# Optimization experiments

Hardware: AMD Instinct MI355X
Metric: run time of the kernel (lower is better)

## Reference

```python
import jax, jax.numpy as jnp
import numpy as np

INPUT_SIZE = 512
HIDDEN_SIZE = 4096
OUTPUT_SIZE = 512
BATCH = 16384

def _xavier_uniform(key, shape):
    fan_out, fan_in = shape
    limit = np.sqrt(6.0 / (fan_in + fan_out)).astype(np.float32)
    return jax.random.uniform(key, shape, jnp.float32, -limit, limit)

def setup_inputs() -> dict:
    key = jax.random.key(0)
    kx, kk, kg = jax.random.split(key, 3)
    x = jax.random.normal(kx, (BATCH, INPUT_SIZE), dtype=jnp.float32)
    kohonen_weights = _xavier_uniform(kk, (HIDDEN_SIZE, INPUT_SIZE))
    grossberg_weights = _xavier_uniform(kg, (OUTPUT_SIZE, HIDDEN_SIZE))
    return {"x": x, "kohonen_weights": kohonen_weights, "grossberg_weights": grossberg_weights}

def reference(x, kohonen_weights, grossberg_weights):
    # cdist (euclidean): sq distances suffice for argmin; sqrt kept for faithfulness
    x_sq = jnp.sum(x * x, axis=1, keepdims=True)                # [B,1]
    w_sq = jnp.sum(kohonen_weights * kohonen_weights, axis=1)   # [H]
    sq = x_sq - 2.0 * (x @ kohonen_weights.T) + w_sq[None, :]   # [B,H]
    distances = jnp.sqrt(jnp.maximum(sq, 0.0))
    winner_indices = jnp.argmin(distances, axis=1)              # [B]
    # one-hot @ grossberg.T == gather rows of grossberg.T
    output = jnp.take(grossberg_weights.T, winner_indices, axis=0)  # [B,O]
    return (output, winner_indices)
```

## Files before the change

kernel.cpp:

```cpp
#include <hip/hip_runtime.h>
#include <cstdint>
#include <cstddef>

#define B_ 16384
#define K_ 512
#define H_ 4096
#define O_ 512

typedef __attribute__((ext_vector_type(4))) float f32x4;
typedef __attribute__((ext_vector_type(8))) short bf16x8;

#define EPS_FLAG 0.125f

__device__ inline unsigned short f32_to_bf16_rne(float f) {
  unsigned u = __float_as_uint(f);
  unsigned r = (u + 0x7fffu + ((u >> 16) & 1u)) >> 16;
  return (unsigned short)r;
}

__device__ float np_pairwise_sumsq512(const float* __restrict__ a) {
  float s[4];
  #pragma unroll
  for (int blk = 0; blk < 4; ++blk) {
    const float* p = a + blk * 128;
    float r[8];
    #pragma unroll
    for (int j = 0; j < 8; ++j) r[j] = __fmul_rn(p[j], p[j]);
    for (int i = 8; i < 128; i += 8) {
      #pragma unroll
      for (int j = 0; j < 8; ++j) r[j] = __fadd_rn(r[j], __fmul_rn(p[i + j], p[i + j]));
    }
    s[blk] = __fadd_rn(__fadd_rn(__fadd_rn(r[0], r[1]), __fadd_rn(r[2], r[3])),
                       __fadd_rn(__fadd_rn(r[4], r[5]), __fadd_rn(r[6], r[7])));
  }
  return __fadd_rn(__fadd_rn(s[0], s[1]), __fadd_rn(s[2], s[3]));
}

__global__ __launch_bounds__(256) void prep_all_kernel(
    const float* __restrict__ x, const float* __restrict__ W,
    const float* __restrict__ G,
    unsigned short* __restrict__ xhi, unsigned short* __restrict__ whi,
    float* __restrict__ xsq, float* __restrict__ wsq, float* __restrict__ GT) {
  const int bid = (int)blockIdx.x;
  const int tid = (int)threadIdx.x;

  if (bid < 2560) {
    const float* src = bid < 2048 ? x : W;
    unsigned short* hi = bid < 2048 ? xhi : whi;
    float* sumsq = bid < 2048 ? xsq : wsq;
    const int r0 = (bid < 2048 ? bid : bid - 2048) * 8;

    __shared__ float buf[8 * 512];
    #pragma unroll
    for (int it = 0; it < 4; ++it) {
      int i = tid + it * 256;
      float4 v = ((const float4*)(src + (size_t)r0 * K_))[i];
      ((float4*)buf)[i] = v;
      ushort4 h;
      h.x = f32_to_bf16_rne(v.x);
      h.y = f32_to_bf16_rne(v.y);
      h.z = f32_to_bf16_rne(v.z);
      h.w = f32_to_bf16_rne(v.w);
      ((ushort4*)(hi + (size_t)r0 * K_))[i] = h;
    }
    __syncthreads();

    const int row = tid >> 5, l = tid & 31, blk = l >> 3, j = l & 7;
    const float* p = buf + row * 512 + blk * 128;
    float r = __fmul_rn(p[j], p[j]);
    #pragma unroll
    for (int i = 8; i < 128; i += 8) r = __fadd_rn(r, __fmul_rn(p[i + j], p[i + j]));
    r = __fadd_rn(r, __shfl_xor(r, 1));
    r = __fadd_rn(r, __shfl_xor(r, 2));
    r = __fadd_rn(r, __shfl_xor(r, 4));
    r = __fadd_rn(r, __shfl_xor(r, 8));
    r = __fadd_rn(r, __shfl_xor(r, 16));
    if (l == 0) sumsq[r0 + row] = r;
  } else {
    __shared__ float t[32][33];
    const int bid2 = bid - 2560;
    const int h0 = (bid2 & 127) * 32, o0 = (bid2 >> 7) * 32;
    const int tx = tid & 31, ty = tid >> 5;
    for (int i = ty; i < 32; i += 8)
      t[i][tx] = G[(size_t)(o0 + i) * H_ + h0 + tx];
    __syncthreads();
    for (int i = ty; i < 32; i += 8)
      GT[(size_t)(h0 + i) * O_ + o0 + tx] = t[tx][i];
  }
}

__global__ void rowsumsq_kernel(const float* __restrict__ src, float* __restrict__ dst,
                                int nrows) {
  int r = blockIdx.x * blockDim.x + threadIdx.x;
  if (r < nrows) dst[r] = np_pairwise_sumsq512(src + (size_t)r * K_);
}

__global__ void transposeG_kernel(const float* __restrict__ G, float* __restrict__ GT) {
  __shared__ float t[32][33];
  int h0 = blockIdx.x * 32, o0 = blockIdx.y * 32;
  for (int i = threadIdx.y; i < 32; i += 8)
    t[i][threadIdx.x] = G[(size_t)(o0 + i) * H_ + h0 + threadIdx.x];
  __syncthreads();
  for (int i = threadIdx.y; i < 32; i += 8)
    GT[(size_t)(h0 + i) * O_ + o0 + threadIdx.x] = t[threadIdx.x][i];
}

__device__ inline void stage_panel256(char* lds_panel, const unsigned short* __restrict__ src,
                                      int rowbase, int kt, int tid) {
  #pragma unroll
  for (int j = 0; j < 4; ++j) {
    int u = j * 512 + tid;
    int row = u >> 3, slot = u & 7;
    const char* g = (const char*)src + (size_t)(rowbase + row) * (K_ * 2) + kt * 128 +
                    ((slot ^ (row & 7)) * 16);
    __builtin_amdgcn_global_load_lds((const __attribute__((address_space(1))) void*)g,
                                     (__attribute__((address_space(3))) void*)(lds_panel + u * 16),
                                     16, 0, 0);
  }
}

__global__ __launch_bounds__(512, 2) void phase1_mfma_kernel(
    const unsigned short* __restrict__ xhi, const unsigned short* __restrict__ whi,
    const float* __restrict__ wsq, const float* __restrict__ xsq,
    float* __restrict__ gmin16 ,
    unsigned short* __restrict__ mk16 ) {
  __shared__ __align__(16) char smem[131072];
  const int tid = (int)threadIdx.x;
  const int wid = tid >> 6, lane = tid & 63;
  const int wr = wid >> 2, wc = wid & 3;
  const int cb = blockIdx.y;
  const int row0 = blockIdx.x * 256, col0 = cb * 256;

  f32x4 acc[8][4];
  #pragma unroll
  for (int i = 0; i < 8; ++i)
    #pragma unroll
    for (int j = 0; j < 4; ++j) acc[i][j] = (f32x4){0.f, 0.f, 0.f, 0.f};

  const int r16 = lane & 15, r7 = lane & 7, sg = lane >> 4;
  const int offK0 = ((sg ^ r7) & 7) * 16;
  const int offK1 = (((4 + sg) ^ r7) & 7) * 16;
  const int arowb = wr * 128 + r16;
  const int browb = wc * 64 + r16;

  stage_panel256(smem, xhi, row0, 0, tid);
  stage_panel256(smem + 32768, whi, col0, 0, tid);
  __syncthreads();

  int buf = 0;
  for (int kt = 0; kt < 8; ++kt) {
    if (kt < 7) {
      stage_panel256(smem + (buf ^ 1) * 65536, xhi, row0, kt + 1, tid);
      stage_panel256(smem + (buf ^ 1) * 65536 + 32768, whi, col0, kt + 1, tid);
    }
    const char* A = smem + buf * 65536;
    const char* Bm = smem + buf * 65536 + 32768;
    #pragma unroll
    for (int ks = 0; ks < 2; ++ks) {
      const int offK = ks ? offK1 : offK0;
      bf16x8 ah[8];
      #pragma unroll
      for (int mf = 0; mf < 8; ++mf)
        ah[mf] = *(const bf16x8*)(A + (arowb + mf * 16) * 128 + offK);
      #pragma unroll
      for (int nf = 0; nf < 4; ++nf) {
        bf16x8 bh = *(const bf16x8*)(Bm + (browb + nf * 16) * 128 + offK);
        #pragma unroll
        for (int mf = 0; mf < 8; ++mf)
          acc[mf][nf] = __builtin_amdgcn_mfma_f32_16x16x32_bf16(ah[mf], bh, acc[mf][nf], 0, 0, 0);
      }
    }
    __syncthreads();
    buf ^= 1;
  }

  float* T = (float*)smem + wid * (16 * 129);
  float* EpiF = (float*)(smem + 66048);
  unsigned short* EpiM = (unsigned short*)(smem + 82432);

  const float xq0 = xsq[row0 + wr * 128 + lane];
  const float xq1 = xsq[row0 + wr * 128 + 64 + lane];
  const int c = r16;

  #pragma unroll
  for (int nf = 0; nf < 4; ++nf) {
    float wq = wsq[col0 + wc * 64 + nf * 16 + c];
    #pragma unroll
    for (int mf = 0; mf < 8; ++mf)
      #pragma unroll
      for (int r = 0; r < 4; ++r)
        T[c * 129 + mf * 16 + sg * 4 + r] = wq - 2.0f * acc[mf][nf][r];
    asm volatile("s_waitcnt lgkmcnt(0)" ::: "memory");
    __builtin_amdgcn_sched_barrier(0);
    #pragma unroll
    for (int half = 0; half < 2; ++half) {
      int lrow = lane + half * 64;
      float xq = half ? xq1 : xq0;
      float v[16];
      #pragma unroll
      for (int c2 = 0; c2 < 16; ++c2) v[c2] = T[c2 * 129 + lrow];
      float mn = v[0];
      #pragma unroll
      for (int c2 = 1; c2 < 16; ++c2) mn = fminf(mn, v[c2]);
      unsigned msk = 0;
      #pragma unroll
      for (int c2 = 0; c2 < 16; ++c2)
        if ((v[c2] <= mn + EPS_FLAG) || (v[c2] + xq <= EPS_FLAG)) msk |= 1u << c2;
      EpiF[(wr * 128 + lrow) * 16 + wc * 4 + nf] = mn;
      EpiM[(wr * 128 + lrow) * 16 + wc * 4 + nf] = (unsigned short)msk;
    }
  }
  __syncthreads();

  {
    int row = tid >> 1, hf = tid & 1;
    const float* fr = EpiF + row * 16 + hf * 8;
    size_t gbase = (size_t)(row0 + row) * 256 + cb * 16 + hf * 8;
    *(float4*)&gmin16[gbase] = *(const float4*)fr;
    *(float4*)&gmin16[gbase + 4] = *(const float4*)(fr + 4);
    uint4 mv = *(const uint4*)(EpiM + row * 16 + hf * 8);
    *(uint4*)&mk16[gbase] = mv;
  }
}

#define P2_ROWS 16
#define P2_CAP 2048

__global__ __launch_bounds__(256) void phase2_block_kernel(
    const float* __restrict__ gm ,
    const unsigned short* __restrict__ mk ,
    const float* __restrict__ x, const float* __restrict__ W,
    const float* __restrict__ xsq, const float* __restrict__ wsq,
    const float* __restrict__ GT, float* __restrict__ out) {
  __shared__ float xls[P2_ROWS * 516];
  __shared__ unsigned short clist[P2_CAP];
  __shared__ unsigned long long bestkey[P2_ROWS];
  __shared__ int ncand;
  const int tid = (int)threadIdx.x;
  const int r = tid >> 4, t16 = tid & 15;
  const int b0 = blockIdx.x * P2_ROWS;
  const int b = b0 + r;

  if (tid < P2_ROWS) bestkey[tid] = 0xFFFFFFFFFFFFFFFFULL;
  if (tid == 0) ncand = 0;

  #pragma unroll
  for (int it = 0; it < 8; ++it) {
    int idx = tid + it * 256;
    int xr = idx >> 7, xw = idx & 127;
    float4 v = ((const float4*)(x + (size_t)(b0 + xr) * K_))[xw];
    *(float4*)&xls[xr * 516 + xw * 4] = v;
  }

  float gv[16];
  #pragma unroll
  for (int j = 0; j < 4; ++j) {
    float4 v = *(const float4*)(gm + (size_t)b * 256 + t16 * 16 + j * 4);
    gv[j * 4 + 0] = v.x;
    gv[j * 4 + 1] = v.y;
    gv[j * 4 + 2] = v.z;
    gv[j * 4 + 3] = v.w;
  }
  unsigned short mv[16];
  #pragma unroll
  for (int j = 0; j < 2; ++j) {
    uint4 u = *(const uint4*)(mk + (size_t)b * 256 + t16 * 16 + j * 8);
    mv[j * 8 + 0] = (unsigned short)(u.x & 0xFFFF);
    mv[j * 8 + 1] = (unsigned short)(u.x >> 16);
    mv[j * 8 + 2] = (unsigned short)(u.y & 0xFFFF);
    mv[j * 8 + 3] = (unsigned short)(u.y >> 16);
    mv[j * 8 + 4] = (unsigned short)(u.z & 0xFFFF);
    mv[j * 8 + 5] = (unsigned short)(u.z >> 16);
    mv[j * 8 + 6] = (unsigned short)(u.w & 0xFFFF);
    mv[j * 8 + 7] = (unsigned short)(u.w >> 16);
  }

  float mn = gv[0];
  #pragma unroll
  for (int j = 1; j < 16; ++j) mn = fminf(mn, gv[j]);
  #pragma unroll
  for (int off = 1; off < 16; off <<= 1) mn = fminf(mn, __shfl_xor(mn, off, 16));
  const float xq = xsq[b];
  const float thr = mn + EPS_FLAG;
  __syncthreads();

  #pragma unroll
  for (int j = 0; j < 16; ++j) {
    float v = gv[j];
    if ((v <= thr) || (v + xq <= EPS_FLAG)) {
      int g = t16 * 16 + j;
      unsigned mbits = mv[j];
      while (mbits) {
        int bit = __ffs(mbits) - 1;
        mbits &= mbits - 1;
        int slot = atomicAdd(&ncand, 1);
        if (slot < P2_CAP)
          clist[slot] = (unsigned short)((r << 12) | (g * 16 + bit));
      }
    }
  }
  __syncthreads();

  int total = ncand;
  if (total <= P2_CAP) {
    for (int i = tid; i < total; i += 256) {
      unsigned e = clist[i];
      int rr = (int)(e >> 12);
      int col = (int)(e & 0xFFF);
      const float* xr = xls + rr * 516;
      const float4* wrow = (const float4*)(W + (size_t)col * K_);
      float acc = 0.0f;
      #pragma unroll 8
      for (int kq = 0; kq < K_ / 4; ++kq) {
        float4 xv = *(const float4*)&xr[kq * 4];
        float4 wv = wrow[kq];
        acc = fmaf(xv.x, wv.x, acc);
        acc = fmaf(xv.y, wv.y, acc);
        acc = fmaf(xv.z, wv.z, acc);
        acc = fmaf(xv.w, wv.w, acc);
      }
      float xqr = xsq[b0 + rr];
      float t2 = xqr - 2.0f * acc;
      float sq = t2 + wsq[col];
      float d = sqrtf(fmaxf(sq, 0.0f));
      unsigned long long key =
          ((unsigned long long)__float_as_uint(d) << 32) | (unsigned)col;
      atomicMin(&bestkey[rr], key);
    }
  } else {
    for (int cc = t16; cc < H_; cc += 16) {
      int g = cc >> 4;
      float gvv = gm[(size_t)b * 256 + g];
      if ((gvv <= thr || gvv + xq <= EPS_FLAG) &&
          ((mk[(size_t)b * 256 + g] >> (cc & 15)) & 1)) {
        const float* xr = xls + r * 516;
        const float4* wrow = (const float4*)(W + (size_t)cc * K_);
        float acc = 0.0f;
        #pragma unroll 8
        for (int kq = 0; kq < K_ / 4; ++kq) {
          float4 xv = *(const float4*)&xr[kq * 4];
          float4 wv = wrow[kq];
          acc = fmaf(xv.x, wv.x, acc);
          acc = fmaf(xv.y, wv.y, acc);
          acc = fmaf(xv.z, wv.z, acc);
          acc = fmaf(xv.w, wv.w, acc);
        }
        float t2 = xq - 2.0f * acc;
        float sq = t2 + wsq[cc];
        float d = sqrtf(fmaxf(sq, 0.0f));
        unsigned long long key =
            ((unsigned long long)__float_as_uint(d) << 32) | (unsigned)cc;
        atomicMin(&bestkey[r], key);
      }
    }
  }
  __syncthreads();

  {
    const unsigned h = (unsigned)(bestkey[r] & 0xFFFFFFFFULL);
    const float4* gsrc = (const float4*)(GT + (size_t)h * O_);
    float4* gdst = (float4*)(out + (size_t)b * O_);
    #pragma unroll
    for (int j = 0; j < 8; ++j) gdst[j * 16 + t16] = gsrc[j * 16 + t16];
    if (t16 == 0) out[(size_t)B_ * O_ + b] = (float)h;
  }
}

#define BM 128
#define BN 128
#define BKK 16

__global__ void init_keys_kernel(unsigned long long* __restrict__ keys) {
  int i = blockIdx.x * blockDim.x + threadIdx.x;
  if (i < B_) keys[i] = 0xFFFFFFFFFFFFFFFFULL;
}

__global__ __launch_bounds__(256) void dist_argmin_kernel(
    const float* __restrict__ x, const float* __restrict__ W,
    const float* __restrict__ xsq, const float* __restrict__ wsq,
    unsigned long long* __restrict__ keys) {
  __shared__ float xs[BKK][BM + 4];
  __shared__ float wsh[BKK][BN + 4];
  const int row0 = blockIdx.x * BM;
  const int col0 = blockIdx.y * BN;
  const int tid = (int)threadIdx.x;
  const int tx = tid & 15, ty = tid >> 4;

  float acc[8][8];
  #pragma unroll
  for (int i = 0; i < 8; ++i)
    #pragma unroll
    for (int j = 0; j < 8; ++j) acc[i][j] = 0.0f;

  for (int kt = 0; kt < K_; kt += BKK) {
    #pragma unroll
    for (int l = 0; l < 2; ++l) {
      int e = tid + l * 256;
      int r = e >> 2, kq = e & 3;
      float4 v = *(const float4*)(x + (size_t)(row0 + r) * K_ + kt + kq * 4);
      xs[kq * 4 + 0][r] = v.x;
      xs[kq * 4 + 1][r] = v.y;
      xs[kq * 4 + 2][r] = v.z;
      xs[kq * 4 + 3][r] = v.w;
      float4 u = *(const float4*)(W + (size_t)(col0 + r) * K_ + kt + kq * 4);
      wsh[kq * 4 + 0][r] = u.x;
      wsh[kq * 4 + 1][r] = u.y;
      wsh[kq * 4 + 2][r] = u.z;
      wsh[kq * 4 + 3][r] = u.w;
    }
    __syncthreads();
    #pragma unroll
    for (int k = 0; k < BKK; ++k) {
      float4 a0 = *(const float4*)&xs[k][ty * 4];
      float4 a1 = *(const float4*)&xs[k][ty * 4 + 64];
      float4 b0 = *(const float4*)&wsh[k][tx * 4];
      float4 b1 = *(const float4*)&wsh[k][tx * 4 + 64];
      float ar[8] = {a0.x, a0.y, a0.z, a0.w, a1.x, a1.y, a1.z, a1.w};
      float br[8] = {b0.x, b0.y, b0.z, b0.w, b1.x, b1.y, b1.z, b1.w};
      #pragma unroll
      for (int i = 0; i < 8; ++i)
        #pragma unroll
        for (int j = 0; j < 8; ++j)
          acc[i][j] = fmaf(ar[i], br[j], acc[i][j]);
    }
    __syncthreads();
  }

  float xv[8], wv[8];
  int rowidx[8], colidx[8];
  #pragma unroll
  for (int i = 0; i < 8; ++i) {
    rowidx[i] = row0 + ty * 4 + (i & 3) + (i >> 2) * 64;
    xv[i] = xsq[rowidx[i]];
  }
  #pragma unroll
  for (int j = 0; j < 8; ++j) {
    colidx[j] = col0 + tx * 4 + (j & 3) + (j >> 2) * 64;
    wv[j] = wsq[colidx[j]];
  }
  #pragma unroll
  for (int i = 0; i < 8; ++i) {
    unsigned long long best = 0xFFFFFFFFFFFFFFFFULL;
    #pragma unroll
    for (int j = 0; j < 8; ++j) {
      float t2 = xv[i] - 2.0f * acc[i][j];
      float sq = t2 + wv[j];
      float d = sqrtf(fmaxf(sq, 0.0f));
      unsigned long long key =
          ((unsigned long long)__float_as_uint(d) << 32) | (unsigned)colidx[j];
      best = key < best ? key : best;
    }
    #pragma unroll
    for (int off = 1; off < 16; off <<= 1) {
      unsigned long long o = __shfl_xor(best, off, 16);
      best = o < best ? o : best;
    }
    if (tx == 0) atomicMin(&keys[rowidx[i]], best);
  }
}

__global__ void finalize_kernel(const unsigned long long* __restrict__ keys,
                                const float* __restrict__ GT,
                                const float* __restrict__ G,
                                float* __restrict__ out, int useGT) {
  int b = blockIdx.x;
  unsigned h = (unsigned)(keys[b] & 0xFFFFFFFFULL);
  if (threadIdx.x == 0) out[(size_t)B_ * O_ + b] = (float)h;
  if (useGT) {
    const float4* src = (const float4*)(GT + (size_t)h * O_);
    float4* dst = (float4*)(out + (size_t)b * O_);
    for (int i = threadIdx.x; i < O_ / 4; i += blockDim.x) dst[i] = src[i];
  } else {
    for (int o = threadIdx.x; o < O_; o += blockDim.x)
      out[(size_t)b * O_ + o] = G[(size_t)o * H_ + h];
  }
}

extern "C" void kernel_launch(void* const* d_in, const int* in_sizes, int n_in,
                              void* d_out, int out_size, void* d_ws, size_t ws_size,
                              hipStream_t stream) {
  const float* x = (const float*)d_in[0];
  const float* W = (const float*)d_in[1];
  const float* G = (const float*)d_in[2];
  float* out = (float*)d_out;
  char* ws = (char*)d_ws;

  size_t o_xsq  = 0;
  size_t o_wsq  = o_xsq + 65536;
  size_t o_xhi  = o_wsq + 16384;
  size_t o_whi  = o_xhi + (size_t)B_ * K_ * 2;
  size_t o_gm   = o_whi + (size_t)H_ * K_ * 2;
  size_t o_mk   = o_gm + (size_t)B_ * 256 * 4;
  size_t o_gt   = o_mk + (size_t)B_ * 256 * 2;
  size_t need   = o_gt + (size_t)H_ * O_ * 4;

  if (ws_size >= need) {
    float* xsq = (float*)(ws + o_xsq);
    float* wsq = (float*)(ws + o_wsq);
    unsigned short* xhi = (unsigned short*)(ws + o_xhi);
    unsigned short* whi = (unsigned short*)(ws + o_whi);
    float* gm = (float*)(ws + o_gm);
    unsigned short* mk = (unsigned short*)(ws + o_mk);
    float* GT = (float*)(ws + o_gt);

    hipLaunchKernelGGL(prep_all_kernel, dim3(2048 + 512 + 2048), dim3(256), 0, stream,
                       x, W, G, xhi, whi, xsq, wsq, GT);
    hipLaunchKernelGGL(phase1_mfma_kernel, dim3(B_ / 256, H_ / 256), dim3(512), 0, stream,
                       xhi, whi, wsq, xsq, gm, mk);
    hipLaunchKernelGGL(phase2_block_kernel, dim3(B_ / P2_ROWS), dim3(256), 0, stream,
                       gm, mk, x, W, xsq, wsq, GT, out);
    return;
  }

  unsigned long long* keys = (unsigned long long*)ws;
  float* xsq = (float*)(ws + 131072);
  float* wsq = (float*)(ws + 131072 + 65536);
  float* GT = (float*)(ws + 131072 + 65536 + 16384);
  size_t base = 131072 + 65536 + 16384;
  int useGT = ws_size >= base + (size_t)H_ * O_ * 4 ? 1 : 0;

  hipLaunchKernelGGL(init_keys_kernel, dim3(B_ / 256), dim3(256), 0, stream, keys);
  hipLaunchKernelGGL(rowsumsq_kernel, dim3(B_ / 256), dim3(256), 0, stream, x, xsq, B_);
  hipLaunchKernelGGL(rowsumsq_kernel, dim3(H_ / 256), dim3(256), 0, stream, W, wsq, H_);
  if (useGT)
    hipLaunchKernelGGL(transposeG_kernel, dim3(H_ / 32, O_ / 32), dim3(32, 8), 0, stream,
                       G, GT);
  hipLaunchKernelGGL(dist_argmin_kernel, dim3(B_ / BM, H_ / BN), dim3(256), 0, stream,
                     x, W, xsq, wsq, keys);
  hipLaunchKernelGGL(finalize_kernel, dim3(B_), dim3(128), 0, stream, keys, GT, G, out,
                     useGT);
}
```

Baseline: 119.4 us.

## Switch coarse distance GEMM from bf16 to scaled fp8 e4m3 MFMA

Quantizes x and W to fp8 e4m3 (W scaled by 64) instead of bf16, halving the bytes staged through LDS and running the phase-1 screening GEMM on fp8 MFMA with four k-steps per 128-byte panel slice. The epilogue rescales the accumulator and the candidate-flag tolerance is widened to absorb the larger quantization error, with exact refinement left to phase 2. This risks more flagged candidates per row, which adds phase-2 refinement work, and relies on the tolerance being wide enough to keep the true argmin.

```diff
diff --git a/kernel.cpp b/kernel.cpp
--- a/kernel.cpp
+++ b/kernel.cpp
@@ -8,47 +8,47 @@
 #define O_ 512
 
 typedef __attribute__((ext_vector_type(4))) float f32x4;
-typedef __attribute__((ext_vector_type(8))) short bf16x8;
-
-#define EPS_FLAG 0.125f
-
-__device__ inline unsigned short f32_to_bf16_rne(float f) {
+
+#define EPS_FLAG 0.75f
+#define WSCALE 64.0f
+#define INV2SCALE 0.03125f
+
+__device__ inline unsigned char f32_to_e4m3(float f) {
   unsigned u = __float_as_uint(f);
-  unsigned r = (u + 0x7fffu + ((u >> 16) & 1u)) >> 16;
-  return (unsigned short)r;
-}
-
-__device__ float np_pairwise_sumsq512(const float* __restrict__ a) {
-  float s[4];
-  #pragma unroll
-  for (int blk = 0; blk < 4; ++blk) {
-    const float* p = a + blk * 128;
-    float r[8];
-    #pragma unroll
-    for (int j = 0; j < 8; ++j) r[j] = __fmul_rn(p[j], p[j]);
-    for (int i = 8; i < 128; i += 8) {
-      #pragma unroll
-      for (int j = 0; j < 8; ++j) r[j] = __fadd_rn(r[j], __fmul_rn(p[i + j], p[i + j]));
-    }
-    s[blk] = __fadd_rn(__fadd_rn(__fadd_rn(r[0], r[1]), __fadd_rn(r[2], r[3])),
-                       __fadd_rn(__fadd_rn(r[4], r[5]), __fadd_rn(r[6], r[7])));
-  }
-  return __fadd_rn(__fadd_rn(s[0], s[1]), __fadd_rn(s[2], s[3]));
+  unsigned char s = (unsigned char)((u >> 24) & 0x80u);
+  if ((u & 0x7FFFFFFFu) == 0) return s;
+  int e = (int)((u >> 23) & 0xFF) - 127;
+  unsigned m = u & 0x7FFFFFu;
+  if (e >= -6) {
+    unsigned keep = m >> 20;
+    unsigned rest = m & 0xFFFFFu;
+    unsigned round = (rest > 0x80000u) || (rest == 0x80000u && (keep & 1u));
+    keep += round;
+    if (keep == 8u) { keep = 0u; e += 1; }
+    if (e > 8) return (unsigned char)(s | 0x7Eu);
+    return (unsigned char)(s | (unsigned)((e + 7) << 3) | keep);
+  } else {
+    float af = __uint_as_float(u & 0x7FFFFFFFu);
+    int q = (int)rintf(af * 512.0f);
+    return (unsigned char)(s | (unsigned)q);
+  }
 }
 
 __global__ __launch_bounds__(256) void prep_all_kernel(
     const float* __restrict__ x, const float* __restrict__ W,
     const float* __restrict__ G,
-    unsigned short* __restrict__ xhi, unsigned short* __restrict__ whi,
+    unsigned char* __restrict__ xq8, unsigned char* __restrict__ wq8,
     float* __restrict__ xsq, float* __restrict__ wsq, float* __restrict__ GT) {
   const int bid = (int)blockIdx.x;
   const int tid = (int)threadIdx.x;
 
   if (bid < 2560) {
-    const float* src = bid < 2048 ? x : W;
-    unsigned short* hi = bid < 2048 ? xhi : whi;
-    float* sumsq = bid < 2048 ? xsq : wsq;
-    const int r0 = (bid < 2048 ? bid : bid - 2048) * 8;
+    const int isx = bid < 2048;
+    const float* src = isx ? x : W;
+    unsigned char* q8 = isx ? xq8 : wq8;
+    float* sumsq = isx ? xsq : wsq;
+    const float scale = isx ? 1.0f : WSCALE;
+    const int r0 = (isx ? bid : bid - 2048) * 8;
 
     __shared__ float buf[8 * 512];
     #pragma unroll
@@ -56,12 +56,12 @@
       int i = tid + it * 256;
       float4 v = ((const float4*)(src + (size_t)r0 * K_))[i];
       ((float4*)buf)[i] = v;
-      ushort4 h;
-      h.x = f32_to_bf16_rne(v.x);
-      h.y = f32_to_bf16_rne(v.y);
-      h.z = f32_to_bf16_rne(v.z);
-      h.w = f32_to_bf16_rne(v.w);
-      ((ushort4*)(hi + (size_t)r0 * K_))[i] = h;
+      uchar4 h;
+      h.x = f32_to_e4m3(v.x * scale);
+      h.y = f32_to_e4m3(v.y * scale);
+      h.z = f32_to_e4m3(v.z * scale);
+      h.w = f32_to_e4m3(v.w * scale);
+      ((uchar4*)(q8 + (size_t)r0 * K_))[i] = h;
     }
     __syncthreads();
 
@@ -89,6 +89,24 @@
   }
 }
 
+__device__ float np_pairwise_sumsq512(const float* __restrict__ a) {
+  float s[4];
+  #pragma unroll
+  for (int blk = 0; blk < 4; ++blk) {
+    const float* p = a + blk * 128;
+    float r[8];
+    #pragma unroll
+    for (int j = 0; j < 8; ++j) r[j] = __fmul_rn(p[j], p[j]);
+    for (int i = 8; i < 128; i += 8) {
+      #pragma unroll
+      for (int j = 0; j < 8; ++j) r[j] = __fadd_rn(r[j], __fmul_rn(p[i + j], p[i + j]));
+    }
+    s[blk] = __fadd_rn(__fadd_rn(__fadd_rn(r[0], r[1]), __fadd_rn(r[2], r[3])),
+                       __fadd_rn(__fadd_rn(r[4], r[5]), __fadd_rn(r[6], r[7])));
+  }
+  return __fadd_rn(__fadd_rn(s[0], s[1]), __fadd_rn(s[2], s[3]));
+}
+
 __global__ void rowsumsq_kernel(const float* __restrict__ src, float* __restrict__ dst,
                                 int nrows) {
   int r = blockIdx.x * blockDim.x + threadIdx.x;
@@ -105,13 +123,13 @@
     GT[(size_t)(h0 + i) * O_ + o0 + threadIdx.x] = t[threadIdx.x][i];
 }
 
-__device__ inline void stage_panel256(char* lds_panel, const unsigned short* __restrict__ src,
-                                      int rowbase, int kt, int tid) {
+__device__ inline void stage_panel_fp8(char* lds_panel, const unsigned char* __restrict__ src,
+                                       int rowbase, int kt, int tid) {
   #pragma unroll
   for (int j = 0; j < 4; ++j) {
     int u = j * 512 + tid;
     int row = u >> 3, slot = u & 7;
-    const char* g = (const char*)src + (size_t)(rowbase + row) * (K_ * 2) + kt * 128 +
+    const char* g = (const char*)src + (size_t)(rowbase + row) * K_ + kt * 128 +
                     ((slot ^ (row & 7)) * 16);
     __builtin_amdgcn_global_load_lds((const __attribute__((address_space(1))) void*)g,
                                      (__attribute__((address_space(3))) void*)(lds_panel + u * 16),
@@ -120,7 +138,7 @@
 }
 
 __global__ __launch_bounds__(512, 2) void phase1_mfma_kernel(
-    const unsigned short* __restrict__ xhi, const unsigned short* __restrict__ whi,
+    const unsigned char* __restrict__ xq8, const unsigned char* __restrict__ wq8,
     const float* __restrict__ wsq, const float* __restrict__ xsq,
     float* __restrict__ gmin16 ,
     unsigned short* __restrict__ mk16 ) {
@@ -138,36 +156,38 @@
     for (int j = 0; j < 4; ++j) acc[i][j] = (f32x4){0.f, 0.f, 0.f, 0.f};
 
   const int r16 = lane & 15, r7 = lane & 7, sg = lane >> 4;
-  const int offK0 = ((sg ^ r7) & 7) * 16;
-  const int offK1 = (((4 + sg) ^ r7) & 7) * 16;
+  int offK[4];
+  #pragma unroll
+  for (int ks = 0; ks < 4; ++ks)
+    offK[ks] = (((2 * ks + (sg >> 1)) ^ r7) & 7) * 16 + (sg & 1) * 8;
   const int arowb = wr * 128 + r16;
   const int browb = wc * 64 + r16;
 
-  stage_panel256(smem, xhi, row0, 0, tid);
-  stage_panel256(smem + 32768, whi, col0, 0, tid);
+  stage_panel_fp8(smem, xq8, row0, 0, tid);
+  stage_panel_fp8(smem + 32768, wq8, col0, 0, tid);
   __syncthreads();
 
   int buf = 0;
-  for (int kt = 0; kt < 8; ++kt) {
-    if (kt < 7) {
-      stage_panel256(smem + (buf ^ 1) * 65536, xhi, row0, kt + 1, tid);
-      stage_panel256(smem + (buf ^ 1) * 65536 + 32768, whi, col0, kt + 1, tid);
+  for (int kt = 0; kt < 4; ++kt) {
+    if (kt < 3) {
+      stage_panel_fp8(smem + (buf ^ 1) * 65536, xq8, row0, kt + 1, tid);
+      stage_panel_fp8(smem + (buf ^ 1) * 65536 + 32768, wq8, col0, kt + 1, tid);
     }
     const char* A = smem + buf * 65536;
     const char* Bm = smem + buf * 65536 + 32768;
     #pragma unroll
-    for (int ks = 0; ks < 2; ++ks) {
-      const int offK = ks ? offK1 : offK0;
-      bf16x8 ah[8];
+    for (int ks = 0; ks < 4; ++ks) {
+      const int ofk = offK[ks];
+      long long ah[8];
       #pragma unroll
       for (int mf = 0; mf < 8; ++mf)
-        ah[mf] = *(const bf16x8*)(A + (arowb + mf * 16) * 128 + offK);
+        ah[mf] = *(const long long*)(A + (arowb + mf * 16) * 128 + ofk);
       #pragma unroll
       for (int nf = 0; nf < 4; ++nf) {
-        bf16x8 bh = *(const bf16x8*)(Bm + (browb + nf * 16) * 128 + offK);
+        long long bh = *(const long long*)(Bm + (browb + nf * 16) * 128 + ofk);
         #pragma unroll
         for (int mf = 0; mf < 8; ++mf)
-          acc[mf][nf] = __builtin_amdgcn_mfma_f32_16x16x32_bf16(ah[mf], bh, acc[mf][nf], 0, 0, 0);
+          acc[mf][nf] = __builtin_amdgcn_mfma_f32_16x16x32_fp8_fp8(ah[mf], bh, acc[mf][nf], 0, 0, 0);
       }
     }
     __syncthreads();
@@ -189,7 +209,7 @@
     for (int mf = 0; mf < 8; ++mf)
       #pragma unroll
       for (int r = 0; r < 4; ++r)
-        T[c * 129 + mf * 16 + sg * 4 + r] = wq - 2.0f * acc[mf][nf][r];
+        T[c * 129 + mf * 16 + sg * 4 + r] = wq - INV2SCALE * acc[mf][nf][r];
     asm volatile("s_waitcnt lgkmcnt(0)" ::: "memory");
     __builtin_amdgcn_sched_barrier(0);
     #pragma unroll
@@ -487,9 +507,9 @@
 
   size_t o_xsq  = 0;
   size_t o_wsq  = o_xsq + 65536;
-  size_t o_xhi  = o_wsq + 16384;
-  size_t o_whi  = o_xhi + (size_t)B_ * K_ * 2;
-  size_t o_gm   = o_whi + (size_t)H_ * K_ * 2;
+  size_t o_xq8  = o_wsq + 16384;
+  size_t o_wq8  = o_xq8 + (size_t)B_ * K_;
+  size_t o_gm   = o_wq8 + (size_t)H_ * K_;
   size_t o_mk   = o_gm + (size_t)B_ * 256 * 4;
   size_t o_gt   = o_mk + (size_t)B_ * 256 * 2;
   size_t need   = o_gt + (size_t)H_ * O_ * 4;
@@ -497,16 +517,16 @@
   if (ws_size >= need) {
     float* xsq = (float*)(ws + o_xsq);
     float* wsq = (float*)(ws + o_wsq);
-    unsigned short* xhi = (unsigned short*)(ws + o_xhi);
-    unsigned short* whi = (unsigned short*)(ws + o_whi);
+    unsigned char* xq8 = (unsigned char*)(ws + o_xq8);
+    unsigned char* wq8 = (unsigned char*)(ws + o_wq8);
     float* gm = (float*)(ws + o_gm);
     unsigned short* mk = (unsigned short*)(ws + o_mk);
     float* GT = (float*)(ws + o_gt);
 
     hipLaunchKernelGGL(prep_all_kernel, dim3(2048 + 512 + 2048), dim3(256), 0, stream,
-                       x, W, G, xhi, whi, xsq, wsq, GT);
+                       x, W, G, xq8, wq8, xsq, wsq, GT);
     hipLaunchKernelGGL(phase1_mfma_kernel, dim3(B_ / 256, H_ / 256), dim3(512), 0, stream,
-                       xhi, whi, wsq, xsq, gm, mk);
+                       xq8, wq8, wsq, xsq, gm, mk);
     hipLaunchKernelGGL(phase2_block_kernel, dim3(B_ / P2_ROWS), dim3(256), 0, stream,
                        gm, mk, x, W, xsq, wsq, GT, out);
     return;
```

After: 190.9 us. +59.8%, slower.

## Pre-pack x into MFMA fragment layout and load A operands directly from global

Applied to the files above, without the earlier changes.

The prep kernel now writes bf16 x in a packed per-fragment order, so each lane of the MFMA kernel can load its A fragments with one contiguous 16-byte global load. The phase-1 kernel drops LDS staging for A and double-buffers only the W panel, cutting LDS to about 90KB. It also removes the min-2-blocks launch bound. The cost is that A loads become direct global loads inside the k-loop, with latency exposed, and occupancy now depends on the register budget.

```diff
diff --git a/kernel.cpp b/kernel.cpp
--- a/kernel.cpp
+++ b/kernel.cpp
@@ -39,29 +39,72 @@
 __global__ __launch_bounds__(256) void prep_all_kernel(
     const float* __restrict__ x, const float* __restrict__ W,
     const float* __restrict__ G,
-    unsigned short* __restrict__ xhi, unsigned short* __restrict__ whi,
+    unsigned short* __restrict__ xpk, unsigned short* __restrict__ whi,
     float* __restrict__ xsq, float* __restrict__ wsq, float* __restrict__ GT) {
   const int bid = (int)blockIdx.x;
   const int tid = (int)threadIdx.x;
-
-  if (bid < 2560) {
-    const float* src = bid < 2048 ? x : W;
-    unsigned short* hi = bid < 2048 ? xhi : whi;
-    float* sumsq = bid < 2048 ? xsq : wsq;
-    const int r0 = (bid < 2048 ? bid : bid - 2048) * 8;
-
-    __shared__ float buf[8 * 512];
+  __shared__ float buf[16 * 516];
+
+  if (bid < 1024) {
+    const int r0 = bid * 16;
+    #pragma unroll
+    for (int it = 0; it < 8; ++it) {
+      int idx = tid + it * 256;
+      int xr = idx >> 7, xw = idx & 127;
+      float4 v = ((const float4*)(x + (size_t)(r0 + xr) * K_))[xw];
+      *(float4*)&buf[xr * 516 + xw * 4] = v;
+    }
+    __syncthreads();
+
+    {
+      const int l = tid & 31, blk = l >> 3, j = l & 7;
+      #pragma unroll
+      for (int hf = 0; hf < 2; ++hf) {
+        int row = (tid >> 5) + hf * 8;
+        const float* p = buf + row * 516 + blk * 128;
+        float r = __fmul_rn(p[j], p[j]);
+        #pragma unroll
+        for (int i = 8; i < 128; i += 8) r = __fadd_rn(r, __fmul_rn(p[i + j], p[i + j]));
+        r = __fadd_rn(r, __shfl_xor(r, 1));
+        r = __fadd_rn(r, __shfl_xor(r, 2));
+        r = __fadd_rn(r, __shfl_xor(r, 4));
+        r = __fadd_rn(r, __shfl_xor(r, 8));
+        r = __fadd_rn(r, __shfl_xor(r, 16));
+        if (l == 0) xsq[r0 + row] = r;
+      }
+    }
+
+    #pragma unroll
+    for (int i = 0; i < 4; ++i) {
+      int s = tid + i * 256;
+      int ks = s >> 6, l = s & 63;
+      const float* p = buf + (l & 15) * 516 + ks * 32 + (l >> 4) * 8;
+      ushort4 lo, hi;
+      lo.x = f32_to_bf16_rne(p[0]);
+      lo.y = f32_to_bf16_rne(p[1]);
+      lo.z = f32_to_bf16_rne(p[2]);
+      lo.w = f32_to_bf16_rne(p[3]);
+      hi.x = f32_to_bf16_rne(p[4]);
+      hi.y = f32_to_bf16_rne(p[5]);
+      hi.z = f32_to_bf16_rne(p[6]);
+      hi.w = f32_to_bf16_rne(p[7]);
+      ushort4* dst = (ushort4*)((char*)xpk + ((size_t)bid * 1024 + s) * 16);
+      dst[0] = lo;
+      dst[1] = hi;
+    }
+  } else if (bid < 1536) {
+    const int r0 = (bid - 1024) * 8;
     #pragma unroll
     for (int it = 0; it < 4; ++it) {
       int i = tid + it * 256;
-      float4 v = ((const float4*)(src + (size_t)r0 * K_))[i];
+      float4 v = ((const float4*)(W + (size_t)r0 * K_))[i];
       ((float4*)buf)[i] = v;
       ushort4 h;
       h.x = f32_to_bf16_rne(v.x);
       h.y = f32_to_bf16_rne(v.y);
       h.z = f32_to_bf16_rne(v.z);
       h.w = f32_to_bf16_rne(v.w);
-      ((ushort4*)(hi + (size_t)r0 * K_))[i] = h;
+      ((ushort4*)(whi + (size_t)r0 * K_))[i] = h;
     }
     __syncthreads();
 
@@ -75,10 +118,10 @@
     r = __fadd_rn(r, __shfl_xor(r, 4));
     r = __fadd_rn(r, __shfl_xor(r, 8));
     r = __fadd_rn(r, __shfl_xor(r, 16));
-    if (l == 0) sumsq[r0 + row] = r;
+    if (l == 0) wsq[r0 + row] = r;
   } else {
-    __shared__ float t[32][33];
-    const int bid2 = bid - 2560;
+    float(*t)[33] = (float(*)[33])buf;
+    const int bid2 = bid - 1536;
     const int h0 = (bid2 & 127) * 32, o0 = (bid2 >> 7) * 32;
     const int tx = tid & 31, ty = tid >> 5;
     for (int i = ty; i < 32; i += 8)
@@ -105,8 +148,8 @@
     GT[(size_t)(h0 + i) * O_ + o0 + threadIdx.x] = t[threadIdx.x][i];
 }
 
-__device__ inline void stage_panel256(char* lds_panel, const unsigned short* __restrict__ src,
-                                      int rowbase, int kt, int tid) {
+__device__ inline void stage_panelB(char* lds_panel, const unsigned short* __restrict__ src,
+                                    int rowbase, int kt, int tid) {
   #pragma unroll
   for (int j = 0; j < 4; ++j) {
     int u = j * 512 + tid;
@@ -119,12 +162,12 @@
   }
 }
 
-__global__ __launch_bounds__(512, 2) void phase1_mfma_kernel(
-    const unsigned short* __restrict__ xhi, const unsigned short* __restrict__ whi,
+__global__ __launch_bounds__(512) void phase1_mfma_kernel(
+    const unsigned short* __restrict__ xpk, const unsigned short* __restrict__ whi,
     const float* __restrict__ wsq, const float* __restrict__ xsq,
     float* __restrict__ gmin16 ,
     unsigned short* __restrict__ mk16 ) {
-  __shared__ __align__(16) char smem[131072];
+  __shared__ __align__(16) char smem[90624];
   const int tid = (int)threadIdx.x;
   const int wid = tid >> 6, lane = tid & 63;
   const int wr = wid >> 2, wc = wid & 3;
@@ -140,34 +183,34 @@
   const int r16 = lane & 15, r7 = lane & 7, sg = lane >> 4;
   const int offK0 = ((sg ^ r7) & 7) * 16;
   const int offK1 = (((4 + sg) ^ r7) & 7) * 16;
-  const int arowb = wr * 128 + r16;
   const int browb = wc * 64 + r16;
-
-  stage_panel256(smem, xhi, row0, 0, tid);
-  stage_panel256(smem + 32768, whi, col0, 0, tid);
+  const char* apk = (const char*)xpk + ((size_t)(blockIdx.x * 16 + wr * 8) * 16 ) * 1024 + lane * 16;
+
+  stage_panelB(smem, whi, col0, 0, tid);
   __syncthreads();
 
   int buf = 0;
   for (int kt = 0; kt < 8; ++kt) {
-    if (kt < 7) {
-      stage_panel256(smem + (buf ^ 1) * 65536, xhi, row0, kt + 1, tid);
-      stage_panel256(smem + (buf ^ 1) * 65536 + 32768, whi, col0, kt + 1, tid);
-    }
-    const char* A = smem + buf * 65536;
-    const char* Bm = smem + buf * 65536 + 32768;
+    if (kt < 7)
+      stage_panelB(smem + (buf ^ 1) * 32768, whi, col0, kt + 1, tid);
+
+    bf16x8 ah[2][8];
+    #pragma unroll
+    for (int ks = 0; ks < 2; ++ks)
+      #pragma unroll
+      for (int mf = 0; mf < 8; ++mf)
+        ah[ks][mf] = *(const bf16x8*)(apk + ((size_t)mf * 16 + (kt * 2 + ks)) * 1024);
+
+    const char* Bm = smem + buf * 32768;
     #pragma unroll
     for (int ks = 0; ks < 2; ++ks) {
       const int offK = ks ? offK1 : offK0;
-      bf16x8 ah[8];
-      #pragma unroll
-      for (int mf = 0; mf < 8; ++mf)
-        ah[mf] = *(const bf16x8*)(A + (arowb + mf * 16) * 128 + offK);
       #pragma unroll
       for (int nf = 0; nf < 4; ++nf) {
         bf16x8 bh = *(const bf16x8*)(Bm + (browb + nf * 16) * 128 + offK);
         #pragma unroll
         for (int mf = 0; mf < 8; ++mf)
-          acc[mf][nf] = __builtin_amdgcn_mfma_f32_16x16x32_bf16(ah[mf], bh, acc[mf][nf], 0, 0, 0);
+          acc[mf][nf] = __builtin_amdgcn_mfma_f32_16x16x32_bf16(ah[ks][mf], bh, acc[mf][nf], 0, 0, 0);
       }
     }
     __syncthreads();
@@ -487,8 +530,8 @@
 
   size_t o_xsq  = 0;
   size_t o_wsq  = o_xsq + 65536;
-  size_t o_xhi  = o_wsq + 16384;
-  size_t o_whi  = o_xhi + (size_t)B_ * K_ * 2;
+  size_t o_xpk  = o_wsq + 16384;
+  size_t o_whi  = o_xpk + (size_t)B_ * K_ * 2;
   size_t o_gm   = o_whi + (size_t)H_ * K_ * 2;
   size_t o_mk   = o_gm + (size_t)B_ * 256 * 4;
   size_t o_gt   = o_mk + (size_t)B_ * 256 * 2;
@@ -497,16 +540,16 @@
   if (ws_size >= need) {
     float* xsq = (float*)(ws + o_xsq);
     float* wsq = (float*)(ws + o_wsq);
-    unsigned short* xhi = (unsigned short*)(ws + o_xhi);
+    unsigned short* xpk = (unsigned short*)(ws + o_xpk);
     unsigned short* whi = (unsigned short*)(ws + o_whi);
     float* gm = (float*)(ws + o_gm);
     unsigned short* mk = (unsigned short*)(ws + o_mk);
     float* GT = (float*)(ws + o_gt);
 
-    hipLaunchKernelGGL(prep_all_kernel, dim3(2048 + 512 + 2048), dim3(256), 0, stream,
-                       x, W, G, xhi, whi, xsq, wsq, GT);
+    hipLaunchKernelGGL(prep_all_kernel, dim3(1024 + 512 + 2048), dim3(256), 0, stream,
+                       x, W, G, xpk, whi, xsq, wsq, GT);
     hipLaunchKernelGGL(phase1_mfma_kernel, dim3(B_ / 256, H_ / 256), dim3(512), 0, stream,
-                       xhi, whi, wsq, xsq, gm, mk);
+                       xpk, whi, wsq, xsq, gm, mk);
     hipLaunchKernelGGL(phase2_block_kernel, dim3(B_ / P2_ROWS), dim3(256), 0, stream,
                        gm, mk, x, W, xsq, wsq, GT, out);
     return;
```

New measurement: 132.3 us. 10.8% more time.
